# Kernel tuning notes

Measured on AMD Instinct MI355X. Metric: run time of the kernel, lower is better.

Reference implementation:

```python
import jax, jax.numpy as jnp
import numpy as np

B, T, D, E, TOP_K = 8, 2048, 512, 8, 2


def setup_inputs() -> dict:
    key = jax.random.key(0)
    ks = jax.random.split(key, 8)
    s = 0.02
    return {
        "x": jax.random.normal(ks[0], (B, T, D), dtype=jnp.float32),
        "eps": jax.random.normal(ks[1], (B, T, E), dtype=jnp.float32),
        "Wr": jax.random.normal(ks[2], (D, E), dtype=jnp.float32) * s,
        "br": jnp.zeros((E,), dtype=jnp.float32),
        "Wn": jax.random.normal(ks[3], (D, E), dtype=jnp.float32) * s,
        "bn": jnp.zeros((E,), dtype=jnp.float32),
        "Wk": jax.random.normal(ks[4], (E, D, D), dtype=jnp.float32) * s,
        "bk": jnp.zeros((E, D), dtype=jnp.float32),
    }


def reference(x, eps, Wr, br, Wn, bn, Wk, bk):
    # Noisy top-k router (NoisyTopkRouter.forward)
    logits = jnp.einsum("btd,de->bte", x, Wr) + br            # [B,T,E]
    noise_logits = jnp.einsum("btd,de->bte", x, Wn) + bn      # [B,T,E]
    noisy = logits + eps * jax.nn.softplus(noise_logits)      # [B,T,E]
    _, top_idx = jax.lax.top_k(noisy, TOP_K)                  # [B,T,k]
    # mask[b,t,e] = True iff expert e is in the token's top-k
    topk_mask = jax.nn.one_hot(top_idx, E, dtype=jnp.float32).sum(-2) > 0
    sparse_logits = jnp.where(topk_mask, noisy, -jnp.inf)
    gating = jax.nn.softmax(sparse_logits, axis=-1)           # zero for non-top-k experts
    # Dense dispatch: every expert's Linear applied to all tokens, then
    # gating (zero outside top-k) selects/scales — same math as the masked
    # gather + per-expert Linear + gating scale in SparseMoE.forward.
    expert_out = jnp.einsum("btd,edh->bteh", x, Wk) + bk      # [B,T,E,D]
    out = jnp.einsum("bte,bteh->bth", gating, expert_out)     # [B,T,D]
    return out
```

## Files before the change

### kernel.cpp

```cpp
#include <hip/hip_runtime.h>
#include <hip/hip_bf16.h>
#include <math.h>

#define B_    8
#define T_    2048
#define NTOK  (B_ * T_)
#define D_    512
#define E_    8
#define NPAIR 28
#define CAP   NTOK

#define RV_TOK    16
#define RV_THR    256
#define XS_STRIDE 132
#define WS_FLOATS 2108

typedef __attribute__((ext_vector_type(4))) float f32x4;
typedef __attribute__((ext_vector_type(8))) short short8;

__device__ __forceinline__ void async_load16(const void* g, void* l) {
    __builtin_amdgcn_global_load_lds(
        (const __attribute__((address_space(1))) unsigned int*)g,
        (__attribute__((address_space(3))) unsigned int*)l,
        16, 0, 0);
}

__global__ __launch_bounds__(256) void transpose_wk(
    const float* __restrict__ Wk, __hip_bfloat16* __restrict__ Wkt)
{
    __shared__ float tile[32][33];
    const int e  = blockIdx.z;
    const int d0 = blockIdx.x * 32;
    const int h0 = blockIdx.y * 32;
    const int tx = threadIdx.x, ty = threadIdx.y;

    const float* src = Wk + ((size_t)e * D_ + d0) * D_ + h0;
    #pragma unroll
    for (int r = ty; r < 32; r += 8)
        tile[r][tx] = src[(size_t)r * D_ + tx];
    __syncthreads();
    __hip_bfloat16* dst = Wkt + ((size_t)e * D_ + h0) * D_ + d0;
    #pragma unroll
    for (int r = ty; r < 32; r += 8)
        dst[(size_t)r * D_ + tx] = __float2bfloat16(tile[tx][r]);
}

__global__ __launch_bounds__(RV_THR) void router_kernel(
    const float* __restrict__ x,
    const float* __restrict__ eps,
    const float* __restrict__ Wr,
    const float* __restrict__ br,
    const float* __restrict__ Wn,
    const float* __restrict__ bn,
    __hip_bfloat16* __restrict__ xb,
    uint4* __restrict__ top2)
{
    __shared__ float xs[RV_TOK * XS_STRIDE];
    __shared__ float wsh[WS_FLOATS];

    const int tid  = threadIdx.x;
    const int tok0 = blockIdx.x * RV_TOK;
    const int lane = tid & 63, wv = tid >> 6;
    const int kidx = lane >> 2, ts = lane & 3;
    const int tl = wv * 4 + ts;
    const int wk = tid >> 1, wh = tid & 1;

    float acc[16];
    #pragma unroll
    for (int c = 0; c < 16; ++c) acc[c] = 0.f;

    for (int kc = 0; kc < D_; kc += 128) {
        #pragma unroll
        for (int it = 0; it < 2; ++it) {
            const int f   = it * RV_THR + tid;
            const int row = f >> 5, col = (f & 31) * 4;
            const f32x4 v = *(const f32x4*)(x + (size_t)(tok0 + row) * D_ + kc + col);
            *(f32x4*)(xs + row * XS_STRIDE + col) = v;
            union { __hip_bfloat16 h[4]; uint2 u; } cv;
            cv.h[0] = __float2bfloat16(v.x); cv.h[1] = __float2bfloat16(v.y);
            cv.h[2] = __float2bfloat16(v.z); cv.h[3] = __float2bfloat16(v.w);
            *(uint2*)(xb + (size_t)(tok0 + row) * D_ + kc + col) = cv.u;
        }
        {
            const float* src = (wh ? Wn : Wr) + (size_t)(kc + wk) * E_;
            const f32x4 w0 = *(const f32x4*)(src);
            const f32x4 w1 = *(const f32x4*)(src + 4);
            float* dst = wsh + wk * 16 + (wk >> 3) * 4 + wh * 8;
            *(f32x4*)(dst)     = w0;
            *(f32x4*)(dst + 4) = w1;
        }
        __syncthreads();

        const float* xra = xs + tl * XS_STRIDE + kidx * 8;
        const f32x4 xa0 = *(const f32x4*)(xra);
        const f32x4 xa1 = *(const f32x4*)(xra + 4);
        const float* wbase = wsh + kidx * 132;
        #pragma unroll
        for (int kk = 0; kk < 8; ++kk) {
            const float xav = (kk < 4) ? xa0[kk] : xa1[kk - 4];
            const float* wrow = wbase + kk * 16;
            #pragma unroll
            for (int c4 = 0; c4 < 4; ++c4) {
                const f32x4 w = *(const f32x4*)(wrow + c4 * 4);
                #pragma unroll
                for (int c = 0; c < 4; ++c)
                    acc[c4 * 4 + c] = fmaf(xav, w[c], acc[c4 * 4 + c]);
            }
        }
        __syncthreads();
    }

    #pragma unroll
    for (int off = 4; off < 64; off <<= 1) {
        #pragma unroll
        for (int c = 0; c < 16; ++c)
            acc[c] += __shfl_xor(acc[c], off);
    }

    if (lane < 4) {
        const int tok = tok0 + tl;
        float nv[8];
        #pragma unroll
        for (int e = 0; e < 8; ++e) {
            const float nl = acc[8 + e] + bn[e];
            const float sp = fmaxf(nl, 0.f) + log1pf(expf(-fabsf(nl)));
            nv[e] = acc[e] + br[e] + eps[(size_t)tok * E_ + e] * sp;
        }
        int i1 = 0; float v1 = nv[0];
        #pragma unroll
        for (int e = 1; e < 8; ++e)
            if (nv[e] > v1) { v1 = nv[e]; i1 = e; }
        int i2 = -1; float v2 = -3.4e38f;
        #pragma unroll
        for (int e = 0; e < 8; ++e)
            if (e != i1 && nv[e] > v2) { v2 = nv[e]; i2 = e; }
        const float t  = expf(v2 - v1);
        const float g1 = 1.f / (1.f + t);
        const float g2 = t / (1.f + t);
        top2[tok] = make_uint4((unsigned)i1 | ((unsigned)i2 << 8),
                               __float_as_uint(g1), __float_as_uint(g2), 0u);
    }
}

__global__ __launch_bounds__(256) void bucket_kernel(
    const uint4* __restrict__ top2,
    int* __restrict__ counts,
    uint4* __restrict__ entries)
{
    __shared__ int hist[NPAIR];
    __shared__ int base[NPAIR];
    const int tid = threadIdx.x;
    const int tok = blockIdx.x * 256 + tid;
    if (tid < NPAIR) hist[tid] = 0;
    __syncthreads();
    const uint4 t = top2[tok];
    const int i1 = t.x & 0xff, i2 = (t.x >> 8) & 0xff;
    const int a = min(i1, i2), b = max(i1, i2);
    const unsigned ga = (i1 < i2) ? t.y : t.z;
    const unsigned gb = (i1 < i2) ? t.z : t.y;
    const int p = a * (15 - a) / 2 + (b - a - 1);
    const int l = atomicAdd(&hist[p], 1);
    __syncthreads();
    if (tid < NPAIR) base[tid] = atomicAdd(counts + tid, hist[tid]);
    __syncthreads();
    entries[(size_t)p * CAP + base[p] + l] = make_uint4((unsigned)tok, ga, gb, 0u);
}

__global__ __launch_bounds__(256, 2) void moe_gemm(
    const __hip_bfloat16* __restrict__ xb,
    const __hip_bfloat16* __restrict__ wkt,
    const float* __restrict__ bk,
    const int* __restrict__ counts,
    const uint4* __restrict__ entries,
    float* __restrict__ out)
{
    constexpr int BM = 128, BN = 128, BK = 32;
    __shared__ __hip_bfloat16 As[BM * BK];
    __shared__ __hip_bfloat16 Bs[2][BN * BK];
    __shared__ uint4 ent[BM];

    const int p  = blockIdx.z;
    const int mt = blockIdx.y;
    const int nt = blockIdx.x;
    const int cnt = counts[p];
    if (mt * BM >= cnt) return;

    int e1 = 0, rem = p;
    while (rem >= 7 - e1) { rem -= 7 - e1; ++e1; }
    const int e2 = e1 + 1 + rem;

    const int tid = threadIdx.x;
    const int wave = tid >> 6, lane = tid & 63;

    if (tid < BM) {
        const int idx = mt * BM + tid;
        ent[tid] = (idx < cnt) ? entries[(size_t)p * CAP + idx]
                               : make_uint4(0u, 0u, 0u, 0u);
    }
    __syncthreads();

    const int quad = lane >> 4, lr = lane & 15;
    const int wm = wave >> 1, wn = wave & 1;
    const int sub = lane >> 2, part = lane & 3;

    f32x4 accA[4][4], accB[4][4];
    #pragma unroll
    for (int i = 0; i < 4; ++i)
        #pragma unroll
        for (int j = 0; j < 4; ++j) {
            accA[i][j] = (f32x4){0.f, 0.f, 0.f, 0.f};
            accB[i][j] = (f32x4){0.f, 0.f, 0.f, 0.f};
        }

    const size_t tok0 = ent[wave * 32 + sub].x;
    const size_t tok1 = ent[wave * 32 + 16 + sub].x;
    const size_t brow1 = (size_t)e1 * D_ + nt * BN + wave * 32 + sub;
    const size_t brow2 = (size_t)e2 * D_ + nt * BN + wave * 32 + sub;

    for (int k0 = 0; k0 < D_; k0 += BK) {
        async_load16(xb + tok0 * D_ + k0 + part * 8, As + (wave * 32) * BK);
        async_load16(xb + tok1 * D_ + k0 + part * 8, As + (wave * 32 + 16) * BK);
        async_load16(wkt + brow1 * D_ + k0 + part * 8, Bs[0] + (wave * 32) * BK);
        async_load16(wkt + (brow1 + 16) * D_ + k0 + part * 8, Bs[0] + (wave * 32 + 16) * BK);
        async_load16(wkt + brow2 * D_ + k0 + part * 8, Bs[1] + (wave * 32) * BK);
        async_load16(wkt + (brow2 + 16) * D_ + k0 + part * 8, Bs[1] + (wave * 32 + 16) * BK);
        __syncthreads();

        short8 a[4], b1[4], b2[4];
        #pragma unroll
        for (int i = 0; i < 4; ++i)
            a[i] = *(const short8*)(As + (wm * 64 + i * 16 + lr) * BK + quad * 8);
        #pragma unroll
        for (int j = 0; j < 4; ++j) {
            b1[j] = *(const short8*)(Bs[0] + (wn * 64 + j * 16 + lr) * BK + quad * 8);
            b2[j] = *(const short8*)(Bs[1] + (wn * 64 + j * 16 + lr) * BK + quad * 8);
        }
        #pragma unroll
        for (int i = 0; i < 4; ++i)
            #pragma unroll
            for (int j = 0; j < 4; ++j) {
                accA[i][j] = __builtin_amdgcn_mfma_f32_16x16x32_bf16(a[i], b1[j], accA[i][j], 0, 0, 0);
                accB[i][j] = __builtin_amdgcn_mfma_f32_16x16x32_bf16(a[i], b2[j], accB[i][j], 0, 0, 0);
            }
        __syncthreads();
    }

    const int colbase = nt * BN + wn * 64 + lr;
    float bkA[4], bkB[4];
    #pragma unroll
    for (int j = 0; j < 4; ++j) {
        bkA[j] = bk[e1 * D_ + colbase + j * 16];
        bkB[j] = bk[e2 * D_ + colbase + j * 16];
    }

    #pragma unroll
    for (int i = 0; i < 4; ++i) {
        #pragma unroll
        for (int r = 0; r < 4; ++r) {
            const int row = wm * 64 + i * 16 + quad * 4 + r;
            if (mt * BM + row < cnt) {
                const uint4 en = ent[row];
                const float ga = __uint_as_float(en.y);
                const float gb = __uint_as_float(en.z);
                float* orow = out + (size_t)en.x * D_ + colbase;
                #pragma unroll
                for (int j = 0; j < 4; ++j)
                    orow[j * 16] = ga * (accA[i][j][r] + bkA[j])
                                 + gb * (accB[i][j][r] + bkB[j]);
            }
        }
    }
}

extern "C" void kernel_launch(void* const* d_in, const int* in_sizes, int n_in,
                              void* d_out, int out_size, void* d_ws, size_t ws_size,
                              hipStream_t stream) {
    const float* x   = (const float*)d_in[0];
    const float* eps = (const float*)d_in[1];
    const float* Wr  = (const float*)d_in[2];
    const float* br  = (const float*)d_in[3];
    const float* Wn  = (const float*)d_in[4];
    const float* bn  = (const float*)d_in[5];
    const float* Wk  = (const float*)d_in[6];
    const float* bk  = (const float*)d_in[7];
    float* out = (float*)d_out;

    char* ws = (char*)d_ws;
    size_t off = 0;
    int* counts = (int*)(ws + off);                     off += 256;
    uint4* entries = (uint4*)(ws + off);                off += (size_t)NPAIR * CAP * 16;
    __hip_bfloat16* xb = (__hip_bfloat16*)(ws + off);   off += (size_t)NTOK * D_ * 2;
    __hip_bfloat16* wkt = (__hip_bfloat16*)(ws + off);  off += (size_t)E_ * D_ * D_ * 2;
    uint4* top2 = (uint4*)(ws + off);                   off += (size_t)NTOK * 16;
    (void)ws_size;

    hipMemsetAsync(counts, 0, NPAIR * sizeof(int), stream);

    transpose_wk<<<dim3(16, 16, E_), dim3(32, 8), 0, stream>>>(Wk, wkt);
    router_kernel<<<dim3(NTOK / RV_TOK), dim3(RV_THR), 0, stream>>>(
        x, eps, Wr, br, Wn, bn, xb, top2);
    bucket_kernel<<<dim3(NTOK / 256), dim3(256), 0, stream>>>(top2, counts, entries);
    moe_gemm<<<dim3(D_ / 128, CAP / 128, NPAIR), dim3(256), 0, stream>>>(
        xb, wkt, bk, counts, entries, out);
}
```

Before: 168.5 us.

## Halve GEMM N-tile, re-split waves along M, and XOR-swizzle LDS layout

The expert GEMM tile shrinks from 128 to 64 output columns, with each wave now owning 32 rows by all 64 columns for both experts. This halves accumulator registers so occupancy can rise to 3 blocks per CU, and it doubles the grid to improve load balance across the pair buckets. A rotation swizzle on the 16-byte chunk index is added to LDS stores and reads to reduce bank conflicts. In exchange, the gathered A rows are reloaded twice as often across N tiles, and each block reuses its A tile across fewer columns.

```diff
diff --git a/kernel.cpp b/kernel.cpp
--- a/kernel.cpp
+++ b/kernel.cpp
@@ -166,7 +166,7 @@
     entries[(size_t)p * CAP + base[p] + l] = make_uint4((unsigned)tok, ga, gb, 0u);
 }
 
-__global__ __launch_bounds__(256, 2) void moe_gemm(
+__global__ __launch_bounds__(256, 3) void moe_gemm(
     const __hip_bfloat16* __restrict__ xb,
     const __hip_bfloat16* __restrict__ wkt,
     const float* __restrict__ bk,
@@ -174,7 +174,7 @@
     const uint4* __restrict__ entries,
     float* __restrict__ out)
 {
-    constexpr int BM = 128, BN = 128, BK = 32;
+    constexpr int BM = 128, BN = 64, BK = 32;
     __shared__ __hip_bfloat16 As[BM * BK];
     __shared__ __hip_bfloat16 Bs[2][BN * BK];
     __shared__ uint4 ent[BM];
@@ -190,7 +190,7 @@
     const int e2 = e1 + 1 + rem;
 
     const int tid = threadIdx.x;
-    const int wave = tid >> 6, lane = tid & 63;
+    const int w = tid >> 6, lane = tid & 63;
 
     if (tid < BM) {
         const int idx = mt * BM + tid;
@@ -200,52 +200,55 @@
     __syncthreads();
 
     const int quad = lane >> 4, lr = lane & 15;
-    const int wm = wave >> 1, wn = wave & 1;
     const int sub = lane >> 2, part = lane & 3;
 
-    f32x4 accA[4][4], accB[4][4];
-    #pragma unroll
-    for (int i = 0; i < 4; ++i)
-        #pragma unroll
-        for (int j = 0; j < 4; ++j) {
-            accA[i][j] = (f32x4){0.f, 0.f, 0.f, 0.f};
-            accB[i][j] = (f32x4){0.f, 0.f, 0.f, 0.f};
-        }
-
-    const size_t tok0 = ent[wave * 32 + sub].x;
-    const size_t tok1 = ent[wave * 32 + 16 + sub].x;
-    const size_t brow1 = (size_t)e1 * D_ + nt * BN + wave * 32 + sub;
-    const size_t brow2 = (size_t)e2 * D_ + nt * BN + wave * 32 + sub;
+    f32x4 acc[2][4][2];
+    #pragma unroll
+    for (int i = 0; i < 2; ++i)
+        #pragma unroll
+        for (int j = 0; j < 4; ++j)
+            #pragma unroll
+            for (int m = 0; m < 2; ++m)
+                acc[i][j][m] = (f32x4){0.f, 0.f, 0.f, 0.f};
+
+    const size_t tokA0 = ent[w * 32 + sub].x;
+    const size_t tokA1 = ent[w * 32 + 16 + sub].x;
+    const int csw = (part - ((sub >> 1) & 3)) & 3;
+    const int mB = w >> 1;
+    const int brow0 = (w & 1) * 32 + sub;
+    const int eb = mB ? e2 : e1;
+    const size_t gB0 = (size_t)eb * D_ + nt * BN + brow0;
 
     for (int k0 = 0; k0 < D_; k0 += BK) {
-        async_load16(xb + tok0 * D_ + k0 + part * 8, As + (wave * 32) * BK);
-        async_load16(xb + tok1 * D_ + k0 + part * 8, As + (wave * 32 + 16) * BK);
-        async_load16(wkt + brow1 * D_ + k0 + part * 8, Bs[0] + (wave * 32) * BK);
-        async_load16(wkt + (brow1 + 16) * D_ + k0 + part * 8, Bs[0] + (wave * 32 + 16) * BK);
-        async_load16(wkt + brow2 * D_ + k0 + part * 8, Bs[1] + (wave * 32) * BK);
-        async_load16(wkt + (brow2 + 16) * D_ + k0 + part * 8, Bs[1] + (wave * 32 + 16) * BK);
+        async_load16(xb + tokA0 * D_ + k0 + csw * 8, As + (w * 32) * BK);
+        async_load16(xb + tokA1 * D_ + k0 + csw * 8, As + (w * 32 + 16) * BK);
+        async_load16(wkt + gB0 * D_ + k0 + csw * 8, Bs[mB] + brow0 * BK - sub * BK + sub * BK);
+        async_load16(wkt + (gB0 + 16) * D_ + k0 + csw * 8,
+                     Bs[mB] + ((w & 1) * 32 + 16) * BK);
         __syncthreads();
 
-        short8 a[4], b1[4], b2[4];
-        #pragma unroll
-        for (int i = 0; i < 4; ++i)
-            a[i] = *(const short8*)(As + (wm * 64 + i * 16 + lr) * BK + quad * 8);
-        #pragma unroll
-        for (int j = 0; j < 4; ++j) {
-            b1[j] = *(const short8*)(Bs[0] + (wn * 64 + j * 16 + lr) * BK + quad * 8);
-            b2[j] = *(const short8*)(Bs[1] + (wn * 64 + j * 16 + lr) * BK + quad * 8);
-        }
-        #pragma unroll
-        for (int i = 0; i < 4; ++i)
+        short8 a[2], b[2][4];
+        const int rsw = (quad + ((lr >> 1) & 3)) & 3;
+        #pragma unroll
+        for (int i = 0; i < 2; ++i)
+            a[i] = *(const short8*)(As + (w * 32 + i * 16 + lr) * BK + rsw * 8);
+        #pragma unroll
+        for (int m = 0; m < 2; ++m)
             #pragma unroll
-            for (int j = 0; j < 4; ++j) {
-                accA[i][j] = __builtin_amdgcn_mfma_f32_16x16x32_bf16(a[i], b1[j], accA[i][j], 0, 0, 0);
-                accB[i][j] = __builtin_amdgcn_mfma_f32_16x16x32_bf16(a[i], b2[j], accB[i][j], 0, 0, 0);
-            }
+            for (int j = 0; j < 4; ++j)
+                b[m][j] = *(const short8*)(Bs[m] + (j * 16 + lr) * BK + rsw * 8);
+        #pragma unroll
+        for (int i = 0; i < 2; ++i)
+            #pragma unroll
+            for (int j = 0; j < 4; ++j)
+                #pragma unroll
+                for (int m = 0; m < 2; ++m)
+                    acc[i][j][m] = __builtin_amdgcn_mfma_f32_16x16x32_bf16(
+                        a[i], b[m][j], acc[i][j][m], 0, 0, 0);
         __syncthreads();
     }
 
-    const int colbase = nt * BN + wn * 64 + lr;
+    const int colbase = nt * BN + lr;
     float bkA[4], bkB[4];
     #pragma unroll
     for (int j = 0; j < 4; ++j) {
@@ -254,10 +257,10 @@
     }
 
     #pragma unroll
-    for (int i = 0; i < 4; ++i) {
+    for (int i = 0; i < 2; ++i) {
         #pragma unroll
         for (int r = 0; r < 4; ++r) {
-            const int row = wm * 64 + i * 16 + quad * 4 + r;
+            const int row = w * 32 + i * 16 + quad * 4 + r;
             if (mt * BM + row < cnt) {
                 const uint4 en = ent[row];
                 const float ga = __uint_as_float(en.y);
@@ -265,8 +268,8 @@
                 float* orow = out + (size_t)en.x * D_ + colbase;
                 #pragma unroll
                 for (int j = 0; j < 4; ++j)
-                    orow[j * 16] = ga * (accA[i][j][r] + bkA[j])
-                                 + gb * (accB[i][j][r] + bkB[j]);
+                    orow[j * 16] = ga * (acc[i][j][0][r] + bkA[j])
+                                 + gb * (acc[i][j][1][r] + bkB[j]);
             }
         }
     }
@@ -300,6 +303,6 @@
     router_kernel<<<dim3(NTOK / RV_TOK), dim3(RV_THR), 0, stream>>>(
         x, eps, Wr, br, Wn, bn, xb, top2);
     bucket_kernel<<<dim3(NTOK / 256), dim3(256), 0, stream>>>(top2, counts, entries);
-    moe_gemm<<<dim3(D_ / 128, CAP / 128, NPAIR), dim3(256), 0, stream>>>(
+    moe_gemm<<<dim3(D_ / 64, CAP / 128, NPAIR), dim3(256), 0, stream>>>(
         xb, wkt, bk, counts, entries, out);
 }
```

New measurement: 172.1 us. 1.02x slower.
